# Optimization experiments

Hardware: AMD Instinct MI355X
Metric: run time of the kernel (lower is better)

The kernel has to match this reference:

```python
import jax, jax.numpy as jnp
import numpy as np

GROUPS = 8
HEADS = 4
EPS = 1e-5


def setup_inputs() -> dict:
    key = jax.random.key(0)
    ks = jax.random.split(key, 5)
    b, c, h, w = 4, 256, 64, 64
    x = jax.random.normal(ks[0], (b, c, h, w), dtype=jnp.float32)
    gn_w = jnp.ones((c,), dtype=jnp.float32)
    gn_b = jnp.zeros((c,), dtype=jnp.float32)
    qkv_w = jax.random.normal(ks[1], (3 * c, c), dtype=jnp.float32) * (c ** -0.5)
    qkv_b = jax.random.normal(ks[2], (3 * c,), dtype=jnp.float32) * 0.01
    proj_w = jax.random.normal(ks[3], (c, c), dtype=jnp.float32) * (c ** -0.5)
    proj_b = jax.random.normal(ks[4], (c,), dtype=jnp.float32) * 0.01
    return {"x": x, "gn_w": gn_w, "gn_b": gn_b, "qkv_w": qkv_w,
            "qkv_b": qkv_b, "proj_w": proj_w, "proj_b": proj_b}


def reference(x, gn_w, gn_b, qkv_w, qkv_b, proj_w, proj_b):
    b, c, h, w = x.shape
    head_dim = c // HEADS
    n = h * w

    # GroupNorm (biased variance, per torch)
    xg = x.reshape(b, GROUPS, c // GROUPS, h, w)
    mean = xg.mean(axis=(2, 3, 4), keepdims=True)
    var = xg.var(axis=(2, 3, 4), keepdims=True)
    xn = ((xg - mean) * jax.lax.rsqrt(var + EPS)).reshape(b, c, h, w)
    xn = xn * gn_w[None, :, None, None] + gn_b[None, :, None, None]

    # 1x1 conv qkv: [b,3c,h,w]
    qkv = jnp.einsum('oc,bchw->bohw', qkv_w, xn) + qkv_b[None, :, None, None]
    # split channel dim as (3, heads, head_dim), flatten spatial -> [b,3,H,d,n]
    qkv = qkv.reshape(b, 3, HEADS, head_dim, n)
    q, k, v = qkv[:, 0], qkv[:, 1], qkv[:, 2]  # each [b,H,d,n]

    scale = head_dim ** -0.5
    attn = jnp.einsum('bhci,bhcj->bhij', q, k) * scale  # [b,H,n,n]
    attn = jax.nn.softmax(attn, axis=-1)
    out = jnp.einsum('bhij,bhcj->bhci', attn, v)  # [b,H,d,n]
    out = out.reshape(b, c, h, w)

    out = jnp.einsum('oc,bchw->bohw', proj_w, out) + proj_b[None, :, None, None]
    return out + x
```

## Files before the change

kernel.cpp:

```cpp
#include <hip/hip_runtime.h>
#include <math.h>

#define NPIX 4096
#define CCH 256

typedef __attribute__((ext_vector_type(4))) float f32x4;
typedef __attribute__((ext_vector_type(8))) short s16x8;
typedef unsigned short u16;

__device__ __forceinline__ short bf16_rne(float x) {
  union { float f; unsigned u; } c; c.f = x;
  unsigned r = c.u + 0x7FFF + ((c.u >> 16) & 1);
  return (short)(r >> 16);
}
__device__ __forceinline__ unsigned cvtpk2(float lo, float hi) {
  unsigned r;
  asm("v_cvt_pk_bf16_f32 %0, %1, %2" : "=v"(r) : "v"(lo), "v"(hi));
  return r;
}
__device__ __forceinline__ unsigned pack2(float a, float b) {
  return cvtpk2(a, b);
}

__device__ __forceinline__ void plane32_swap(unsigned& a, unsigned& b) {
#if __has_builtin(__builtin_amdgcn_permlane32_swap)
  auto r = __builtin_amdgcn_permlane32_swap(a, b, false, false);
  a = r[0]; b = r[1];
#else
  asm("s_nop 2\n\tv_permlane32_swap_b32 %0, %1\n\ts_nop 2" : "+v"(a), "+v"(b));
#endif
}
__device__ __forceinline__ void plane16_swap(unsigned& a, unsigned& b) {
#if __has_builtin(__builtin_amdgcn_permlane16_swap)
  auto r = __builtin_amdgcn_permlane16_swap(a, b, false, false);
  a = r[0]; b = r[1];
#else
  asm("s_nop 2\n\tv_permlane16_swap_b32 %0, %1\n\ts_nop 2" : "+v"(a), "+v"(b));
#endif
}

__device__ __forceinline__ float red_max_cross(float x) {
  unsigned a = __float_as_uint(x), b = a;
  plane32_swap(a, b);
  float m = fmaxf(__uint_as_float(a), __uint_as_float(b));
  a = __float_as_uint(m); b = a;
  plane16_swap(a, b);
  return fmaxf(__uint_as_float(a), __uint_as_float(b));
}
__device__ __forceinline__ float red_sum_cross(float x) {
  unsigned a = __float_as_uint(x), b = a;
  plane32_swap(a, b);
  float m = __uint_as_float(a) + __uint_as_float(b);
  a = __float_as_uint(m); b = a;
  plane16_swap(a, b);
  return __uint_as_float(a) + __uint_as_float(b);
}

#define QSCALE 0.18033688011f

__global__ __launch_bounds__(256) void gn_stats_part(
    const float* __restrict__ x, double2* __restrict__ partials)
{
  const int blk = blockIdx.x;
  const int bg = blk >> 3, chunk = blk & 7;
  const float4* base = (const float4*)(x + (size_t)bg * 131072 + (size_t)chunk * 16384);
  double s = 0.0, ss = 0.0;
  for (int idx = threadIdx.x; idx < 4096; idx += 256) {
    float4 v = base[idx];
    s  += (double)v.x + (double)v.y + (double)v.z + (double)v.w;
    ss += (double)v.x * v.x + (double)v.y * v.y + (double)v.z * v.z + (double)v.w * v.w;
  }
  __shared__ double rs[256], rss[256];
  rs[threadIdx.x] = s; rss[threadIdx.x] = ss;
  __syncthreads();
  for (int off = 128; off > 0; off >>= 1) {
    if (threadIdx.x < off) { rs[threadIdx.x] += rs[threadIdx.x + off]; rss[threadIdx.x] += rss[threadIdx.x + off]; }
    __syncthreads();
  }
  if (threadIdx.x == 0) {
    double2 p; p.x = rs[0]; p.y = rss[0];
    partials[blk] = p;
  }
}

__global__ __launch_bounds__(256) void wcvt_kernel(
    const float* __restrict__ qkv_w, const float* __restrict__ proj_w, const float* __restrict__ qkv_b,
    const double2* __restrict__ partials, const float* __restrict__ gn_w, const float* __restrict__ gn_b,
    u16* __restrict__ wq, u16* __restrict__ wp, float* __restrict__ biasq,
    float* __restrict__ alpha, float* __restrict__ beta)
{
  int idx = blockIdx.x * 256 + threadIdx.x;
  if (idx < 196608) {
    float v = qkv_w[idx];
    if (idx < 65536) v *= QSCALE;
    wq[idx] = (u16)bf16_rne(v);
  } else {
    int j = idx - 196608;
    wp[j] = (u16)bf16_rne(proj_w[j]);
  }
  if (idx < 768) {
    float bv = qkv_b[idx];
    if (idx < 256) bv *= QSCALE;
    biasq[idx] = bv;
  }
  if (blockIdx.x == 0) {
    __shared__ float sm[32], sr[32];
    const int tid = threadIdx.x;
    if (tid < 32) {
      double s = 0.0, ss = 0.0;
      for (int c = 0; c < 8; ++c) { double2 p = partials[tid * 8 + c]; s += p.x; ss += p.y; }
      double mean = s / 131072.0;
      double var  = ss / 131072.0 - mean * mean;
      sm[tid] = (float)mean;
      sr[tid] = (float)(1.0 / sqrt(var + 1e-5));
    }
    __syncthreads();
#pragma unroll
    for (int p = 0; p < 4; ++p) {
      int e = p * 256 + tid;
      int ch = e & 255;
      int bg = (e >> 8) * 8 + (ch >> 5);
      float a = sr[bg] * gn_w[ch];
      alpha[e] = a;
      beta[e]  = gn_b[ch] - sm[bg] * a;
    }
  }
}

__global__ __launch_bounds__(256) void gn_apply_t_kernel(
    const float* __restrict__ x, const float* __restrict__ alpha, const float* __restrict__ beta,
    u16* __restrict__ Xt)
{
  const int b = blockIdx.z, c0 = blockIdx.y * 64, n0 = blockIdx.x * 64;
  const int tid = threadIdx.x;
  __shared__ u16 T[64 * 68];
  const int n4 = (tid & 15) * 4, cr = tid >> 4;
#pragma unroll
  for (int p = 0; p < 4; ++p) {
    int cl = cr + 16 * p;
    int c = c0 + cl;
    float a = alpha[b * CCH + c], bt = beta[b * CCH + c];
    float4 v = *(const float4*)&x[((size_t)b * CCH + c) * NPIX + n0 + n4];
    T[(n4 + 0) * 68 + cl] = (u16)bf16_rne(v.x * a + bt);
    T[(n4 + 1) * 68 + cl] = (u16)bf16_rne(v.y * a + bt);
    T[(n4 + 2) * 68 + cl] = (u16)bf16_rne(v.z * a + bt);
    T[(n4 + 3) * 68 + cl] = (u16)bf16_rne(v.w * a + bt);
  }
  __syncthreads();
#pragma unroll
  for (int it = 0; it < 2; ++it) {
    int linear = it * 256 + tid;
    int n = linear >> 3, ch = linear & 7;
    s16x8 v = *(const s16x8*)&T[n * 68 + ch * 8];
    *(s16x8*)&Xt[((size_t)b * NPIX + n0 + n) * CCH + c0 + ch * 8] = v;
  }
}

__global__ __launch_bounds__(256) void qkv_gemm_kernel(
    const u16* __restrict__ Wbf, const float* __restrict__ biasv, const u16* __restrict__ Xt,
    u16* __restrict__ Qt, u16* __restrict__ Kt, u16* __restrict__ Vb)
{
  const int nblk = blockIdx.x, m0 = blockIdx.y * 64;
  const int tid = threadIdx.x, wave = tid >> 6, lane = tid & 63;
  const int n16 = lane & 15, quad = lane >> 4;
  const int n0 = nblk * 128 + wave * 32;

  f32x4 acc[4][2];
#pragma unroll
  for (int a = 0; a < 4; ++a)
#pragma unroll
    for (int c = 0; c < 2; ++c) acc[a][c] = (f32x4){0.f, 0.f, 0.f, 0.f};

#pragma unroll
  for (int k0 = 0; k0 < 256; k0 += 32) {
    s16x8 af[4], bfr[2];
#pragma unroll
    for (int msub = 0; msub < 4; ++msub)
      af[msub] = *(const s16x8*)&Wbf[(size_t)(m0 + msub * 16 + n16) * 256 + k0 + quad * 8];
#pragma unroll
    for (int nsub = 0; nsub < 2; ++nsub)
      bfr[nsub] = *(const s16x8*)&Xt[(size_t)(n0 + nsub * 16 + n16) * 256 + k0 + quad * 8];
#pragma unroll
    for (int msub = 0; msub < 4; ++msub)
#pragma unroll
      for (int nsub = 0; nsub < 2; ++nsub)
        acc[msub][nsub] = __builtin_amdgcn_mfma_f32_16x16x32_bf16(af[msub], bfr[nsub], acc[msub][nsub], 0, 0, 0);
  }

  __shared__ u16 T[8704];
  if (m0 < 512) {
#pragma unroll
    for (int msub = 0; msub < 4; ++msub)
#pragma unroll
      for (int nsub = 0; nsub < 2; ++nsub) {
        float b0 = biasv[m0 + msub * 16 + quad * 4 + 0];
        float b1 = biasv[m0 + msub * 16 + quad * 4 + 1];
        float b2 = biasv[m0 + msub * 16 + quad * 4 + 2];
        float b3 = biasv[m0 + msub * 16 + quad * 4 + 3];
        uint2 w2;
        w2.x = pack2(acc[msub][nsub][0] + b0, acc[msub][nsub][1] + b1);
        w2.y = pack2(acc[msub][nsub][2] + b2, acc[msub][nsub][3] + b3);
        *(uint2*)&T[(wave * 32 + nsub * 16 + n16) * 68 + msub * 16 + quad * 4] = w2;
      }
    __syncthreads();
    u16* dst = (m0 < 256) ? Qt : Kt;
    const int coff = m0 & 255;
#pragma unroll
    for (int it = 0; it < 4; ++it) {
      int linear = it * 256 + tid;
      int n = linear >> 3, ch = linear & 7;
      s16x8 v = *(const s16x8*)&T[n * 68 + ch * 8];
      *(s16x8*)&dst[(size_t)(nblk * 128 + n) * 256 + coff + ch * 8] = v;
    }
  } else {
#pragma unroll
    for (int msub = 0; msub < 4; ++msub)
#pragma unroll
      for (int nsub = 0; nsub < 2; ++nsub) {
        int ncol = wave * 32 + nsub * 16 + n16;
#pragma unroll
        for (int r = 0; r < 4; ++r) {
          int m = msub * 16 + quad * 4 + r;
          T[m * 136 + ncol] = (u16)bf16_rne(acc[msub][nsub][r] + biasv[m0 + m]);
        }
      }
    __syncthreads();
    const int b = (nblk * 128) >> 12, i0n = (nblk * 128) & 4095;
#pragma unroll
    for (int it = 0; it < 4; ++it) {
      int linear = it * 256 + tid;
      int mloc = linear >> 4, ch = linear & 15;
      s16x8 v = *(const s16x8*)&T[mloc * 136 + ch * 8];
      int c = (m0 - 512) + mloc;
      *(s16x8*)&Vb[((size_t)b * CCH + c) * NPIX + i0n + ch * 8] = v;
    }
  }
}

__device__ __forceinline__ void kv_load(
    const u16* __restrict__ Kb, const u16* __restrict__ Vg, int h, int j0, int sj, int part,
    s16x8& k0, s16x8& k1, s16x8& v0, s16x8& v1)
{
  const s16x8* kp = (const s16x8*)&Kb[(size_t)(j0 + sj) * 256 + h * 64 + part * 16];
  const s16x8* vp = (const s16x8*)&Vg[(size_t)sj * NPIX + j0 + part * 16];
  k0 = kp[0]; k1 = kp[1]; v0 = vp[0]; v1 = vp[1];
}
__device__ __forceinline__ void kv_store(
    u16* Ksb, u16* Vsb, int sbase, int rr0,
    s16x8 k0, s16x8 k1, s16x8 v0, s16x8 v1)
{
  *(s16x8*)&Ksb[sbase + (rr0 + 0) * 128] = k0;
  *(s16x8*)&Ksb[sbase + (rr0 + 1) * 128] = k1;
  *(s16x8*)&Vsb[sbase + (rr0 + 0) * 128] = v0;
  *(s16x8*)&Vsb[sbase + (rr0 + 1) * 128] = v1;
}

__device__ __forceinline__ void attn_tile(
    const u16* Ksb, const u16* Vsb, const s16x8 qf[2], int lane,
    f32x4 ot[4], float& m_i, float& l_i)
{
  f32x4 st[4];
#pragma unroll
  for (int a = 0; a < 4; ++a) st[a] = (f32x4){0.f, 0.f, 0.f, 0.f};
  __builtin_amdgcn_s_setprio(1);
#pragma unroll
  for (int ks = 0; ks < 2; ++ks)
#pragma unroll
    for (int jsub = 0; jsub < 4; ++jsub) {
      s16x8 a = *(const s16x8*)&Ksb[(jsub * 2 + ks) * 520 + lane * 8];
      st[jsub] = __builtin_amdgcn_mfma_f32_16x16x32_bf16(a, qf[ks], st[jsub], 0, 0, 0);
    }
  __builtin_amdgcn_s_setprio(0);

  float t0 = fmaxf(fmaxf(st[0][0], st[0][1]), fmaxf(st[0][2], st[0][3]));
  float t1 = fmaxf(fmaxf(st[1][0], st[1][1]), fmaxf(st[1][2], st[1][3]));
  float t2 = fmaxf(fmaxf(st[2][0], st[2][1]), fmaxf(st[2][2], st[2][3]));
  float t3 = fmaxf(fmaxf(st[3][0], st[3][1]), fmaxf(st[3][2], st[3][3]));
  float tm = fmaxf(fmaxf(t0, t1), fmaxf(t2, t3));
  tm = red_max_cross(tm);

  if (__any(tm > m_i + 8.0f)) {
    float mn = fmaxf(m_i, tm);
    float al = __builtin_amdgcn_exp2f(m_i - mn);
    m_i = mn;
    l_i *= al;
#pragma unroll
    for (int dsub = 0; dsub < 4; ++dsub)
#pragma unroll
      for (int r = 0; r < 4; ++r) ot[dsub][r] *= al;
  }

#pragma unroll
  for (int jsub = 0; jsub < 4; ++jsub)
#pragma unroll
    for (int r = 0; r < 4; ++r)
      st[jsub][r] = __builtin_amdgcn_exp2f(st[jsub][r] - m_i);

  float s0 = (st[0][0] + st[0][1]) + (st[0][2] + st[0][3]);
  float s1 = (st[1][0] + st[1][1]) + (st[1][2] + st[1][3]);
  float s2 = (st[2][0] + st[2][1]) + (st[2][2] + st[2][3]);
  float s3 = (st[3][0] + st[3][1]) + (st[3][2] + st[3][3]);
  float ps = (s0 + s1) + (s2 + s3);
  ps = red_sum_cross(ps);
  l_i += ps;

  s16x8 pb[2];
#pragma unroll
  for (int ks = 0; ks < 2; ++ks) {
    unsigned a0 = cvtpk2(st[2 * ks][0], st[2 * ks][1]);
    unsigned a1 = cvtpk2(st[2 * ks][2], st[2 * ks][3]);
    unsigned b0 = cvtpk2(st[2 * ks + 1][0], st[2 * ks + 1][1]);
    unsigned b1 = cvtpk2(st[2 * ks + 1][2], st[2 * ks + 1][3]);
    plane32_swap(a0, b0);
    plane16_swap(a0, b0);
    plane32_swap(a1, b1);
    plane16_swap(a1, b1);
    union { unsigned u[4]; s16x8 v; } pu;
    pu.u[0] = a0; pu.u[1] = a1; pu.u[2] = b0; pu.u[3] = b1;
    pb[ks] = pu.v;
  }

  __builtin_amdgcn_s_setprio(1);
#pragma unroll
  for (int ks = 0; ks < 2; ++ks)
#pragma unroll
    for (int dsub = 0; dsub < 4; ++dsub) {
      s16x8 a = *(const s16x8*)&Vsb[(dsub * 2 + ks) * 520 + lane * 8];
      ot[dsub] = __builtin_amdgcn_mfma_f32_16x16x32_bf16(a, pb[ks], ot[dsub], 0, 0, 0);
    }
  __builtin_amdgcn_s_setprio(0);
}

__global__ __launch_bounds__(256, 4) void attn_kernel4(
    const u16* __restrict__ Qt, const u16* __restrict__ Kt,
    const u16* __restrict__ Vb, u16* __restrict__ Ot)
{
  const int b = blockIdx.z, h = blockIdx.y;
  const int tid = threadIdx.x;
  const int wave = tid >> 6, lane = tid & 63;
  const int n16 = lane & 15, quad = lane >> 4;
  const int i0w = blockIdx.x * 64 + wave * 16;

  __shared__ u16 Ks[2][8 * 520];
  __shared__ u16 Vs[2][8 * 520];

  const u16* Qb = Qt + (size_t)b * NPIX * 256;
  const u16* Kb = Kt + (size_t)b * NPIX * 256;
  const u16* Vg = Vb + ((size_t)b * CCH + h * 64) * NPIX;

  s16x8 qf[2];
#pragma unroll
  for (int ks = 0; ks < 2; ++ks)
    qf[ks] = *(const s16x8*)&Qb[(size_t)(i0w + n16) * 256 + h * 64 + ks * 32 + quad * 8];

  f32x4 ot[4];
#pragma unroll
  for (int a = 0; a < 4; ++a) ot[a] = (f32x4){0.f, 0.f, 0.f, 0.f};
  float m_i = -1e30f;
  float l_i = 0.f;

  const int sj = tid >> 2;
  const int part = tid & 3;
  const int sh = part >> 1;
  const int rr0 = (part & 1) * 2;
  const int sbase = ((sj >> 4) * 2 + sh) * 520 + (sj & 15) * 8;

  s16x8 k0, k1, v0, v1;

  kv_load(Kb, Vg, h, 0, sj, part, k0, k1, v0, v1);
  kv_store(Ks[0], Vs[0], sbase, rr0, k0, k1, v0, v1);
  __syncthreads();

#pragma unroll 1
  for (int t = 0; t < 62; t += 2) {
    kv_load(Kb, Vg, h, (t + 1) * 64, sj, part, k0, k1, v0, v1);
    attn_tile(Ks[0], Vs[0], qf, lane, ot, m_i, l_i);
    kv_store(Ks[1], Vs[1], sbase, rr0, k0, k1, v0, v1);
    __syncthreads();
    kv_load(Kb, Vg, h, (t + 2) * 64, sj, part, k0, k1, v0, v1);
    attn_tile(Ks[1], Vs[1], qf, lane, ot, m_i, l_i);
    kv_store(Ks[0], Vs[0], sbase, rr0, k0, k1, v0, v1);
    __syncthreads();
  }
  kv_load(Kb, Vg, h, 63 * 64, sj, part, k0, k1, v0, v1);
  attn_tile(Ks[0], Vs[0], qf, lane, ot, m_i, l_i);
  kv_store(Ks[1], Vs[1], sbase, rr0, k0, k1, v0, v1);
  __syncthreads();
  attn_tile(Ks[1], Vs[1], qf, lane, ot, m_i, l_i);

  float rl = 1.0f / l_i;
#pragma unroll
  for (int dsub = 0; dsub < 4; ++dsub) {
    uint2 w2;
    w2.x = cvtpk2(ot[dsub][0] * rl, ot[dsub][1] * rl);
    w2.y = cvtpk2(ot[dsub][2] * rl, ot[dsub][3] * rl);
    size_t addr = (size_t)((size_t)b * NPIX + i0w + n16) * 256 + h * 64 + dsub * 16 + quad * 4;
    *(uint2*)&Ot[addr] = w2;
  }
}

__global__ __launch_bounds__(256) void proj_gemm_kernel(
    const u16* __restrict__ Wp, const float* __restrict__ proj_b, const u16* __restrict__ Ot,
    const float* __restrict__ x, float* __restrict__ out)
{
  const int nblk = blockIdx.x, m0 = blockIdx.y * 64;
  const int tid = threadIdx.x, wave = tid >> 6, lane = tid & 63;
  const int n16 = lane & 15, quad = lane >> 4;
  const int n0 = nblk * 128 + wave * 32;

  f32x4 acc[4][2];
#pragma unroll
  for (int a = 0; a < 4; ++a)
#pragma unroll
    for (int c = 0; c < 2; ++c) acc[a][c] = (f32x4){0.f, 0.f, 0.f, 0.f};

#pragma unroll
  for (int k0 = 0; k0 < 256; k0 += 32) {
    s16x8 af[4], bfr[2];
#pragma unroll
    for (int msub = 0; msub < 4; ++msub)
      af[msub] = *(const s16x8*)&Wp[(size_t)(m0 + msub * 16 + n16) * 256 + k0 + quad * 8];
#pragma unroll
    for (int nsub = 0; nsub < 2; ++nsub)
      bfr[nsub] = *(const s16x8*)&Ot[(size_t)(n0 + nsub * 16 + n16) * 256 + k0 + quad * 8];
#pragma unroll
    for (int msub = 0; msub < 4; ++msub)
#pragma unroll
      for (int nsub = 0; nsub < 2; ++nsub)
        acc[msub][nsub] = __builtin_amdgcn_mfma_f32_16x16x32_bf16(af[msub], bfr[nsub], acc[msub][nsub], 0, 0, 0);
  }

  __shared__ float T[64 * 132];
#pragma unroll
  for (int msub = 0; msub < 4; ++msub)
#pragma unroll
    for (int nsub = 0; nsub < 2; ++nsub) {
      int ncol = wave * 32 + nsub * 16 + n16;
#pragma unroll
      for (int r = 0; r < 4; ++r) {
        int m = msub * 16 + quad * 4 + r;
        T[m * 132 + ncol] = acc[msub][nsub][r];
      }
    }
  __syncthreads();
  const int b = (nblk * 128) >> 12, i0n = (nblk * 128) & 4095;
#pragma unroll
  for (int it = 0; it < 8; ++it) {
    int linear = it * 256 + tid;
    int m = linear >> 5, ch = linear & 31;
    f32x4 v = *(const f32x4*)&T[m * 132 + ch * 4];
    float bs = proj_b[m0 + m];
    size_t g = ((size_t)b * CCH + m0 + m) * NPIX + i0n + ch * 4;
    float4 rv = *(const float4*)&x[g];
    float4 o;
    o.x = v[0] + bs + rv.x; o.y = v[1] + bs + rv.y;
    o.z = v[2] + bs + rv.z; o.w = v[3] + bs + rv.w;
    *(float4*)&out[g] = o;
  }
}

extern "C" void kernel_launch(void* const* d_in, const int* in_sizes, int n_in,
                              void* d_out, int out_size, void* d_ws, size_t ws_size,
                              hipStream_t stream)
{
  const float* x      = (const float*)d_in[0];
  const float* gn_w   = (const float*)d_in[1];
  const float* gn_b   = (const float*)d_in[2];
  const float* qkv_w  = (const float*)d_in[3];
  const float* qkv_b  = (const float*)d_in[4];
  const float* proj_w = (const float*)d_in[5];
  const float* proj_b = (const float*)d_in[6];
  float* out = (float*)d_out;

  float* ws    = (float*)d_ws;
  float* alpha = ws;
  float* beta  = ws + 1024;
  float* biasq = ws + 2048;
  double2* partials = (double2*)(ws + 2816);
  u16*   wq    = (u16*)(ws + 4096);
  u16*   wp    = (u16*)(ws + 102400);
  u16*   Xt    = (u16*)(ws + 135168);
  u16*   Qt    = (u16*)(ws + 2232320);
  u16*   Kt    = (u16*)(ws + 4329472);
  u16*   Vb    = (u16*)(ws + 6426624);
  u16*   Ot    = (u16*)(ws + 8523776);

  gn_stats_part<<<256, 256, 0, stream>>>(x, partials);
  wcvt_kernel<<<1024, 256, 0, stream>>>(qkv_w, proj_w, qkv_b, partials, gn_w, gn_b,
                                        wq, wp, biasq, alpha, beta);
  gn_apply_t_kernel<<<dim3(64, 4, 4), 256, 0, stream>>>(x, alpha, beta, Xt);
  qkv_gemm_kernel<<<dim3(128, 12), 256, 0, stream>>>(wq, biasq, Xt, Qt, Kt, Vb);
  attn_kernel4<<<dim3(64, 4, 4), 256, 0, stream>>>(Qt, Kt, Vb, Ot);
  proj_gemm_kernel<<<dim3(128, 4), 256, 0, stream>>>(wp, proj_b, Ot, x, out);
}
```

Measured before the change: 256.3 us.

## Split attention KV range in two halves and merge with combine kernel

```diff
diff --git a/kernel.cpp b/kernel.cpp
--- a/kernel.cpp
+++ b/kernel.cpp
@@ -20,6 +20,14 @@
 }
 __device__ __forceinline__ unsigned pack2(float a, float b) {
   return cvtpk2(a, b);
+}
+__device__ __forceinline__ float max3f(float a, float b, float c) {
+  float d;
+  asm("v_max3_f32 %0, %1, %2, %3" : "=v"(d) : "v"(a), "v"(b), "v"(c));
+  return d;
+}
+__device__ __forceinline__ float bf16_to_f32(unsigned short v) {
+  return __uint_as_float(((unsigned)v) << 16);
 }
 
 __device__ __forceinline__ void plane32_swap(unsigned& a, unsigned& b) {
@@ -272,11 +280,14 @@
     }
   __builtin_amdgcn_s_setprio(0);
 
-  float t0 = fmaxf(fmaxf(st[0][0], st[0][1]), fmaxf(st[0][2], st[0][3]));
-  float t1 = fmaxf(fmaxf(st[1][0], st[1][1]), fmaxf(st[1][2], st[1][3]));
-  float t2 = fmaxf(fmaxf(st[2][0], st[2][1]), fmaxf(st[2][2], st[2][3]));
-  float t3 = fmaxf(fmaxf(st[3][0], st[3][1]), fmaxf(st[3][2], st[3][3]));
-  float tm = fmaxf(fmaxf(t0, t1), fmaxf(t2, t3));
+  float m0 = max3f(st[0][0], st[0][1], st[0][2]);
+  float m1 = max3f(st[0][3], st[1][0], st[1][1]);
+  float m2 = max3f(st[1][2], st[1][3], st[2][0]);
+  float m3 = max3f(st[2][1], st[2][2], st[2][3]);
+  float m4 = max3f(st[3][0], st[3][1], st[3][2]);
+  float m5 = max3f(m0, m1, st[3][3]);
+  float m6 = max3f(m2, m3, m4);
+  float tm = fmaxf(m5, m6);
   tm = red_max_cross(tm);
 
   if (__any(tm > m_i + 8.0f)) {
@@ -331,18 +342,21 @@
   __builtin_amdgcn_s_setprio(0);
 }
 
-__global__ __launch_bounds__(256, 4) void attn_kernel4(
+__global__ __launch_bounds__(256, 8) void attn_kernel5(
     const u16* __restrict__ Qt, const u16* __restrict__ Kt,
-    const u16* __restrict__ Vb, u16* __restrict__ Ot)
+    const u16* __restrict__ Vb, u16* __restrict__ P0, u16* __restrict__ P1,
+    float* __restrict__ mlbuf)
 {
   const int b = blockIdx.z, h = blockIdx.y;
+  const int xb = blockIdx.x;
+  const int half = xb >> 6, iblk = xb & 63;
   const int tid = threadIdx.x;
   const int wave = tid >> 6, lane = tid & 63;
   const int n16 = lane & 15, quad = lane >> 4;
-  const int i0w = blockIdx.x * 64 + wave * 16;
-
-  __shared__ u16 Ks[2][8 * 520];
-  __shared__ u16 Vs[2][8 * 520];
+  const int i0w = iblk * 64 + wave * 16;
+
+  __shared__ u16 Ks[8 * 520];
+  __shared__ u16 Vs[8 * 520];
 
   const u16* Qb = Qt + (size_t)b * NPIX * 256;
   const u16* Kb = Kt + (size_t)b * NPIX * 256;
@@ -364,38 +378,65 @@
   const int sh = part >> 1;
   const int rr0 = (part & 1) * 2;
   const int sbase = ((sj >> 4) * 2 + sh) * 520 + (sj & 15) * 8;
+  const int jbase = half * 2048;
 
   s16x8 k0, k1, v0, v1;
 
-  kv_load(Kb, Vg, h, 0, sj, part, k0, k1, v0, v1);
-  kv_store(Ks[0], Vs[0], sbase, rr0, k0, k1, v0, v1);
-  __syncthreads();
-
 #pragma unroll 1
-  for (int t = 0; t < 62; t += 2) {
-    kv_load(Kb, Vg, h, (t + 1) * 64, sj, part, k0, k1, v0, v1);
-    attn_tile(Ks[0], Vs[0], qf, lane, ot, m_i, l_i);
-    kv_store(Ks[1], Vs[1], sbase, rr0, k0, k1, v0, v1);
+  for (int t = 0; t < 32; ++t) {
+    kv_load(Kb, Vg, h, jbase + t * 64, sj, part, k0, k1, v0, v1);
     __syncthreads();
-    kv_load(Kb, Vg, h, (t + 2) * 64, sj, part, k0, k1, v0, v1);
-    attn_tile(Ks[1], Vs[1], qf, lane, ot, m_i, l_i);
-    kv_store(Ks[0], Vs[0], sbase, rr0, k0, k1, v0, v1);
+    kv_store(Ks, Vs, sbase, rr0, k0, k1, v0, v1);
     __syncthreads();
-  }
-  kv_load(Kb, Vg, h, 63 * 64, sj, part, k0, k1, v0, v1);
-  attn_tile(Ks[0], Vs[0], qf, lane, ot, m_i, l_i);
-  kv_store(Ks[1], Vs[1], sbase, rr0, k0, k1, v0, v1);
-  __syncthreads();
-  attn_tile(Ks[1], Vs[1], qf, lane, ot, m_i, l_i);
+    attn_tile(Ks, Vs, qf, lane, ot, m_i, l_i);
+  }
 
   float rl = 1.0f / l_i;
+  u16* dst = (half == 0) ? P0 : P1;
 #pragma unroll
   for (int dsub = 0; dsub < 4; ++dsub) {
     uint2 w2;
     w2.x = cvtpk2(ot[dsub][0] * rl, ot[dsub][1] * rl);
     w2.y = cvtpk2(ot[dsub][2] * rl, ot[dsub][3] * rl);
     size_t addr = (size_t)((size_t)b * NPIX + i0w + n16) * 256 + h * 64 + dsub * 16 + quad * 4;
-    *(uint2*)&Ot[addr] = w2;
+    *(uint2*)&dst[addr] = w2;
+  }
+  if (quad == 0) {
+    int idx = half * 65536 + b * 16384 + h * 4096 + i0w + n16;
+    float2 ml; ml.x = m_i; ml.y = l_i;
+    *(float2*)&mlbuf[idx * 2] = ml;
+  }
+}
+
+__global__ __launch_bounds__(256) void combine_kernel(
+    const u16* __restrict__ P0, u16* __restrict__ Ot, const float* __restrict__ mlbuf)
+{
+  const int t = threadIdx.x;
+  const int r = blockIdx.x * 32 + (t >> 3);
+  const int seg = t & 7;
+  const int b = r >> 12, i = r & 4095;
+  const int h = seg >> 1;
+  const int idx = b * 16384 + h * 4096 + i;
+  float2 ml0 = *(const float2*)&mlbuf[(size_t)idx * 2];
+  float2 ml1 = *(const float2*)&mlbuf[(size_t)(65536 + idx) * 2];
+  float m = fmaxf(ml0.x, ml1.x);
+  float c0 = ml0.y * __builtin_amdgcn_exp2f(ml0.x - m);
+  float c1 = ml1.y * __builtin_amdgcn_exp2f(ml1.x - m);
+  float rn = 1.0f / (c0 + c1);
+  float w0 = c0 * rn, w1 = c1 * rn;
+  size_t base = (size_t)r * 256 + seg * 32;
+#pragma unroll
+  for (int p = 0; p < 4; ++p) {
+    s16x8 a = *(const s16x8*)&P0[base + p * 8];
+    s16x8 c = *(const s16x8*)&Ot[base + p * 8];
+    union { unsigned u[4]; s16x8 v; } o;
+#pragma unroll
+    for (int e = 0; e < 4; ++e) {
+      float lo = w0 * bf16_to_f32((unsigned short)a[2 * e])     + w1 * bf16_to_f32((unsigned short)c[2 * e]);
+      float hi = w0 * bf16_to_f32((unsigned short)a[2 * e + 1]) + w1 * bf16_to_f32((unsigned short)c[2 * e + 1]);
+      o.u[e] = cvtpk2(lo, hi);
+    }
+    *(s16x8*)&Ot[base + p * 8] = o.v;
   }
 }
 
@@ -484,12 +525,16 @@
   u16*   Kt    = (u16*)(ws + 4329472);
   u16*   Vb    = (u16*)(ws + 6426624);
   u16*   Ot    = (u16*)(ws + 8523776);
+  float* mlbuf = ws + 10620928;
+
+  u16* P0 = Xt;
 
   gn_stats_part<<<256, 256, 0, stream>>>(x, partials);
   wcvt_kernel<<<1024, 256, 0, stream>>>(qkv_w, proj_w, qkv_b, partials, gn_w, gn_b,
                                         wq, wp, biasq, alpha, beta);
   gn_apply_t_kernel<<<dim3(64, 4, 4), 256, 0, stream>>>(x, alpha, beta, Xt);
   qkv_gemm_kernel<<<dim3(128, 12), 256, 0, stream>>>(wq, biasq, Xt, Qt, Kt, Vb);
-  attn_kernel4<<<dim3(64, 4, 4), 256, 0, stream>>>(Qt, Kt, Vb, Ot);
+  attn_kernel5<<<dim3(128, 4, 4), 256, 0, stream>>>(Qt, Kt, Vb, P0, Ot, mlbuf);
+  combine_kernel<<<512, 256, 0, stream>>>(P0, Ot, mlbuf);
   proj_gemm_kernel<<<dim3(128, 4), 256, 0, stream>>>(wp, proj_b, Ot, x, out);
 }
```

Result: no change. 257.5 us (+0.5%).
